# Performance work log

Hardware: AMD Instinct MI355X
Metric: run time of the kernel (lower is better)

## Reference

```python
import jax, jax.numpy as jnp
import numpy as np

B, N, C, K, S = 2, 20000, 64, 16, 4  # batch, points, channels, neighbors, share_planes
CS = C // S
EPS = 1e-5


def _gather(x, idx):
    # x: [B, C, N], idx: [B, N, K] -> [B, C, N, K]
    return jax.vmap(lambda xb, ib: xb[:, ib])(x, idx)


def _bn(x, g, b, m, v):
    # inference-mode BatchNorm2d over channel axis 1; x: [B, C, N, K]
    scale = (g / jnp.sqrt(v + EPS))[None, :, None, None]
    return (x - m[None, :, None, None]) * scale + b[None, :, None, None]


def setup_inputs() -> dict:
    key = jax.random.key(0)
    ks = jax.random.split(key, 32)
    d = {}
    d["coord"] = jax.random.normal(ks[0], (B, N, 3), jnp.float32)
    d["q"] = jax.random.normal(ks[1], (B, C, N), jnp.float32)
    d["k"] = jax.random.normal(ks[2], (B, C, N), jnp.float32)
    d["neighbor_indices"] = jax.random.randint(ks[3], (B, N, K), 0, N, jnp.int32)
    sc = 1.0 / np.sqrt(C)
    d["wq"] = jax.random.normal(ks[4], (C, C), jnp.float32) * sc
    d["bq"] = jnp.zeros((C,), jnp.float32)
    d["wk"] = jax.random.normal(ks[5], (C, C), jnp.float32) * sc
    d["bk"] = jnp.zeros((C,), jnp.float32)
    d["wv"] = jax.random.normal(ks[6], (C, C), jnp.float32) * sc
    d["bv"] = jnp.zeros((C,), jnp.float32)
    # linear_p: Conv2d(3,3,1) -> BN(3) -> ReLU -> Conv2d(3,C,1)
    d["p1_w"] = jax.random.normal(ks[7], (3, 3), jnp.float32) * 0.5
    d["p1_b"] = jnp.zeros((3,), jnp.float32)
    d["p_bn_g"] = jnp.ones((3,), jnp.float32)
    d["p_bn_b"] = jnp.zeros((3,), jnp.float32)
    d["p_bn_m"] = jax.random.normal(ks[8], (3,), jnp.float32) * 0.1
    d["p_bn_v"] = jax.random.uniform(ks[9], (3,), jnp.float32) + 0.5
    d["p2_w"] = jax.random.normal(ks[10], (C, 3), jnp.float32) * 0.5
    d["p2_b"] = jnp.zeros((C,), jnp.float32)
    # linear_w: BN(C) -> ReLU -> Conv2d(C, C//S, 1) -> BN(C//S) -> ReLU -> Conv2d(C//S, C//S, 1)
    d["w_bn1_g"] = jnp.ones((C,), jnp.float32)
    d["w_bn1_b"] = jnp.zeros((C,), jnp.float32)
    d["w_bn1_m"] = jax.random.normal(ks[11], (C,), jnp.float32) * 0.1
    d["w_bn1_v"] = jax.random.uniform(ks[12], (C,), jnp.float32) + 0.5
    d["w1_w"] = jax.random.normal(ks[13], (CS, C), jnp.float32) * sc
    d["w1_b"] = jnp.zeros((CS,), jnp.float32)
    d["w_bn2_g"] = jnp.ones((CS,), jnp.float32)
    d["w_bn2_b"] = jnp.zeros((CS,), jnp.float32)
    d["w_bn2_m"] = jax.random.normal(ks[14], (CS,), jnp.float32) * 0.1
    d["w_bn2_v"] = jax.random.uniform(ks[15], (CS,), jnp.float32) + 0.5
    d["w2_w"] = jax.random.normal(ks[16], (CS, CS), jnp.float32) / np.sqrt(CS)
    d["w2_b"] = jnp.zeros((CS,), jnp.float32)
    return d


def reference(coord, q, k, neighbor_indices, wq, bq, wk, bk, wv, bv,
              p1_w, p1_b, p_bn_g, p_bn_b, p_bn_m, p_bn_v, p2_w, p2_b,
              w_bn1_g, w_bn1_b, w_bn1_m, w_bn1_v, w1_w, w1_b,
              w_bn2_g, w_bn2_b, w_bn2_m, w_bn2_v, w2_w, w2_b):
    # 1x1 Conv1d projections: [B, C, N]
    x_q = jnp.einsum('oc,bcn->bon', wq, q) + bq[None, :, None]
    x_k = jnp.einsum('oc,bcn->bon', wk, k) + bk[None, :, None]
    x_v = jnp.einsum('oc,bcn->bon', wv, q) + bv[None, :, None]
    # KNN gathers -> [B, *, N, K]
    p_r = _gather(jnp.swapaxes(coord, 1, 2), neighbor_indices)  # [B, 3, N, K]
    x_k = _gather(x_k, neighbor_indices)                        # [B, C, N, K]
    x_v = _gather(x_v, neighbor_indices)                        # [B, C, N, K]
    # positional MLP
    p_r = jnp.einsum('oc,bcnk->bonk', p1_w, p_r) + p1_b[None, :, None, None]
    p_r = jax.nn.relu(_bn(p_r, p_bn_g, p_bn_b, p_bn_m, p_bn_v))
    p_r = jnp.einsum('oc,bcnk->bonk', p2_w, p_r) + p2_b[None, :, None, None]  # [B, C, N, K]
    # attention weights MLP
    w = x_k - x_q[:, :, :, None] + p_r                          # [B, C, N, K]
    w = jax.nn.relu(_bn(w, w_bn1_g, w_bn1_b, w_bn1_m, w_bn1_v))
    w = jnp.einsum('oc,bcnk->bonk', w1_w, w) + w1_b[None, :, None, None]      # [B, C/S, N, K]
    w = jax.nn.relu(_bn(w, w_bn2_g, w_bn2_b, w_bn2_m, w_bn2_v))
    w = jnp.einsum('oc,bcnk->bonk', w2_w, w) + w2_b[None, :, None, None]
    w = jax.nn.softmax(w, axis=-1)                              # softmax over K
    # grouped weighted sum
    v = jnp.transpose(x_v + p_r, (0, 2, 3, 1)).reshape(B, N, K, S, CS)  # [B, N, K, S, C/S]
    wp = jnp.transpose(w, (0, 2, 3, 1))                                  # [B, N, K, C/S]
    x = jnp.einsum('bnksg,bnkg->bnsg', v, wp).reshape(B, N, C)
    return jnp.transpose(x, (0, 2, 1))  # [B, C, N]
```

## Files before the change

kernel.cpp:

```cpp
#include <hip/hip_runtime.h>
#include <hip/hip_bf16.h>
#include <math.h>

#define B_ 2
#define N_ 20000
#define C_ 64
#define K_ 16
#define CS_ 16
#define EPS_ 1e-5f

typedef float f32x4_t  __attribute__((ext_vector_type(4)));
typedef short bf16x8_t __attribute__((ext_vector_type(8)));
typedef short bf16x4_t __attribute__((ext_vector_type(4)));

__device__ __forceinline__ unsigned int packbf2(float a, float b)
{
    union { __hip_bfloat162 h; unsigned int u; } cv;
    cv.h = __float22bfloat162_rn(float2{a, b});
    return cv.u;
}
__device__ __forceinline__ float bf_lo(unsigned int w)
{
    return __builtin_bit_cast(float, w << 16);
}
__device__ __forceinline__ float bf_hi(unsigned int w)
{
    return __builtin_bit_cast(float, w & 0xFFFF0000u);
}
__device__ __forceinline__ void wave_fence()
{
    __builtin_amdgcn_wave_barrier();
}

__device__ __forceinline__ float row_sum16(float x)
{
    float s = x;
    s += __builtin_bit_cast(float, __builtin_amdgcn_update_dpp(
            0, __builtin_bit_cast(int, s), 0x128, 0xF, 0xF, false));
    s += __builtin_bit_cast(float, __builtin_amdgcn_update_dpp(
            0, __builtin_bit_cast(int, s), 0x124, 0xF, 0xF, false));
    s += __builtin_bit_cast(float, __builtin_amdgcn_update_dpp(
            0, __builtin_bit_cast(int, s), 0x122, 0xF, 0xF, false));
    s += __builtin_bit_cast(float, __builtin_amdgcn_update_dpp(
            0, __builtin_bit_cast(int, s), 0x121, 0xF, 0xF, false));
    return s;
}

__global__ __launch_bounds__(256) void setup_kernel(
    const float* __restrict__ wq, const float* __restrict__ wk,
    const float* __restrict__ wv,
    const float* __restrict__ bq, const float* __restrict__ bk,
    const float* __restrict__ bv,
    const float* __restrict__ w1_w, const float* __restrict__ w1_b,
    const float* __restrict__ w2_w, const float* __restrict__ w2_b,
    const float* __restrict__ w_bn1_g, const float* __restrict__ w_bn1_b,
    const float* __restrict__ w_bn1_m, const float* __restrict__ w_bn1_v,
    const float* __restrict__ w_bn2_g, const float* __restrict__ w_bn2_b,
    const float* __restrict__ w_bn2_m, const float* __restrict__ w_bn2_v,
    const float* __restrict__ p2_w, const float* __restrict__ p2_b,
    uint4* __restrict__ wtab, uint4* __restrict__ a1tab,
    uint2* __restrict__ a2tab, float* __restrict__ cz,
    float4* __restrict__ ctab, float4* __restrict__ ptab)
{
    const int t   = threadIdx.x;
    const int blk = blockIdx.x;
    {
        int e = blk * 256 + t;
        int m = e >> 9, rem = e & 511;
        int og = rem >> 7, half = (rem >> 6) & 1, l = rem & 63;
        const float* W = (m == 0) ? wq : ((m == 1) ? wk : wv);
        const float* base = W + (size_t)(og * 16 + (l & 15)) * C_ + half * 32 + (l >> 4) * 8;
        uint4 o;
        o.x = packbf2(base[0], base[1]); o.y = packbf2(base[2], base[3]);
        o.z = packbf2(base[4], base[5]); o.w = packbf2(base[6], base[7]);
        wtab[e] = o;
    }
    if (blk == 0 && t < 128) {
        int half = t >> 6, l = t & 63;
        const float* base = w1_w + (size_t)(l & 15) * C_ + half * 32 + (l >> 4) * 8;
        uint4 o;
        o.x = packbf2(base[0], base[1]); o.y = packbf2(base[2], base[3]);
        o.z = packbf2(base[4], base[5]); o.w = packbf2(base[6], base[7]);
        a1tab[t] = o;
    }
    if (blk == 1 && t < 64) {
        const float* base = w2_w + (t & 15) * 16 + (t >> 4) * 4;
        uint2 o;
        o.x = packbf2(base[0], base[1]); o.y = packbf2(base[2], base[3]);
        a2tab[t] = o;
    }
    if (blk == 2 && t < 16) {
        float s = w_bn2_g[t] * rsqrtf(w_bn2_v[t] + EPS_);
        cz[t]      = s;
        cz[16 + t] = (w1_b[t] - w_bn2_m[t]) * s + w_bn2_b[t];
        cz[32 + t] = w2_b[t];
    }
    if (blk == 3 && t < 64) {
        float s   = w_bn1_g[t] * rsqrtf(w_bn1_v[t] + EPS_);
        float b1f = w_bn1_b[t] - w_bn1_m[t] * s;
        ctab[t] = float4{s, s * bq[t] - b1f, bk[t], bv[t]};
    }
    if (blk == 4 && t < 64) {
        ptab[t] = float4{p2_w[t*3+0], p2_w[t*3+1], p2_w[t*3+2], p2_b[t]};
    }
}

__global__ __launch_bounds__(256) void proj_kernel(
    const float* __restrict__ q, const float* __restrict__ kin,
    const float* __restrict__ coord,
    const float* __restrict__ p1_w, const float* __restrict__ p1_b,
    const float* __restrict__ p_bn_g, const float* __restrict__ p_bn_b,
    const float* __restrict__ p_bn_m, const float* __restrict__ p_bn_v,
    const uint4* __restrict__ wtab,
    const float4* __restrict__ ctab, const float4* __restrict__ ptab,
    unsigned int* __restrict__ xq2, unsigned int* __restrict__ kv_t)
{
    constexpr int PS = 26;
    __shared__ unsigned int qp[32 * PS];
    __shared__ unsigned int kp[32 * PS];

    const int t   = threadIdx.x;
    const int og  = __builtin_amdgcn_readfirstlane(t >> 6);
    const int l   = t & 63;
    const int col = l & 15;
    const int qd  = l >> 4;
    const int pt0 = blockIdx.x * 16;
    const int pt  = pt0 + col;
    const int b   = pt0 / N_;
    const int n   = pt - b * N_;
    const size_t cb = (size_t)b * C_ * N_ + n;

#pragma unroll
    for (int r = 0; r < 2; r++) {
        int cp = (og << 3) + (qd << 1) + r;
        int ci = cp * 2;
        float q0 = q[cb + (size_t)ci * N_];
        float q1 = q[cb + (size_t)(ci + 1) * N_];
        float k0 = kin[cb + (size_t)ci * N_];
        float k1 = kin[cb + (size_t)(ci + 1) * N_];
        qp[cp * PS + col] = packbf2(q0, q1);
        kp[cp * PS + col] = packbf2(k0, k1);
    }

    union bf8u { bf16x8_t v; uint4 u4; };
    bf8u awq[2], awk[2], awv[2];
#pragma unroll
    for (int half = 0; half < 2; half++) {
        awq[half].u4 = wtab[0 * 512 + og * 128 + half * 64 + l];
        awk[half].u4 = wtab[1 * 512 + og * 128 + half * 64 + l];
        awv[half].u4 = wtab[2 * 512 + og * 128 + half * 64 + l];
    }

    __syncthreads();

    union bf8b { bf16x8_t v; unsigned int u[4]; };
    bf8b bq_[2], bk_[2];
#pragma unroll
    for (int half = 0; half < 2; half++) {
#pragma unroll
        for (int i2 = 0; i2 < 4; i2++) {
            int cp = half * 16 + qd * 4 + i2;
            bq_[half].u[i2] = qp[cp * PS + col];
            bk_[half].u[i2] = kp[cp * PS + col];
        }
    }

    f32x4_t uq = {0.f, 0.f, 0.f, 0.f};
    f32x4_t uv = {0.f, 0.f, 0.f, 0.f};
    f32x4_t uk = {0.f, 0.f, 0.f, 0.f};
    uq = __builtin_amdgcn_mfma_f32_16x16x32_bf16(awq[0].v, bq_[0].v, uq, 0, 0, 0);
    uq = __builtin_amdgcn_mfma_f32_16x16x32_bf16(awq[1].v, bq_[1].v, uq, 0, 0, 0);
    uv = __builtin_amdgcn_mfma_f32_16x16x32_bf16(awv[0].v, bq_[0].v, uv, 0, 0, 0);
    uv = __builtin_amdgcn_mfma_f32_16x16x32_bf16(awv[1].v, bq_[1].v, uv, 0, 0, 0);
    uk = __builtin_amdgcn_mfma_f32_16x16x32_bf16(awk[0].v, bk_[0].v, uk, 0, 0, 0);
    uk = __builtin_amdgcn_mfma_f32_16x16x32_bf16(awk[1].v, bk_[1].v, uk, 0, 0, 0);

    float pbs[3], pbb[3];
#pragma unroll
    for (int j = 0; j < 3; j++) {
        float s = p_bn_g[j] * rsqrtf(p_bn_v[j] + EPS_);
        pbs[j] = s;
        pbb[j] = (p1_b[j] - p_bn_m[j]) * s + p_bn_b[j];
    }
    float cx = coord[pt * 3 + 0], cy = coord[pt * 3 + 1], cz = coord[pt * 3 + 2];
    float h0 = fmaxf(0.f, (p1_w[0]*cx + p1_w[1]*cy + p1_w[2]*cz) * pbs[0] + pbb[0]);
    float h1 = fmaxf(0.f, (p1_w[3]*cx + p1_w[4]*cy + p1_w[5]*cz) * pbs[1] + pbb[1]);
    float h2 = fmaxf(0.f, (p1_w[6]*cx + p1_w[7]*cy + p1_w[8]*cz) * pbs[2] + pbb[2]);

    const int ch0 = og * 16 + qd * 4;
    float xv2[4];
    uint4 kvo;
#pragma unroll
    for (int rr = 0; rr < 4; rr++) {
        const float4 ct  = ctab[ch0 + rr];
        const float4 pt4 = ptab[ch0 + rr];
        float pos = fmaf(pt4.x, h0, fmaf(pt4.y, h1, fmaf(pt4.z, h2, pt4.w)));
        xv2[rr]   = fmaf(ct.x, uq[rr], ct.y);
        float kk  = ct.x * (uk[rr] + ct.z + pos);
        float vv  = uv[rr] + ct.w + pos;
        (&kvo.x)[rr] = packbf2(kk, vv);
    }
    uint2 xqo;
    xqo.x = packbf2(xv2[0], xv2[1]);
    xqo.y = packbf2(xv2[2], xv2[3]);
    *reinterpret_cast<uint2*>(xq2 + (size_t)pt * 32 + (ch0 >> 1)) = xqo;
    *reinterpret_cast<uint4*>(kv_t + (size_t)pt * C_ + ch0) = kvo;
}

#define WROW 72
#define WPN  (K_ * WROW)
#define SS4  20
#define SPN  (K_ * SS4)
#define OS   68

__global__ __launch_bounds__(512, 8) void attn_kernel(
    const int* __restrict__ nbr,
    const unsigned int* __restrict__ xq2, const unsigned int* __restrict__ kv_t,
    const uint4* __restrict__ a1tab, const uint2* __restrict__ a2tab,
    const float* __restrict__ cz,
    float* __restrict__ out)
{
    __shared__ unsigned short wlds_all[8 * WPN];
    __shared__ float          sfb_all[8 * SPN];
    __shared__ float          otile[8 * OS];

    const int t  = threadIdx.x;
    const int w  = __builtin_amdgcn_readfirstlane(t >> 6);
    const int l  = t & 63;
    const int al = l & 15;
    const int qd = l >> 4;
    const int cquad = al;
    const int kq    = qd;
    const int c0    = cquad * 4;
    const int g0    = c0 & 15;

    const int pt0 = blockIdx.x * 8;
    const int b   = pt0 / N_;
    const int bB  = b * N_;
    const int bn  = pt0 + w;

    unsigned short* wlds = wlds_all + w * WPN;
    float*          sfb  = sfb_all + w * SPN;

    const int* nb = nbr + (size_t)bn * K_;
    uint4 kvw[4];
#pragma unroll
    for (int j = 0; j < 4; j++) {
        int idx = nb[kq * 4 + j];
        kvw[j] = *reinterpret_cast<const uint4*>(kv_t + ((size_t)(bB + idx) * C_ + c0));
    }
    const uint2 xqu = *reinterpret_cast<const uint2*>(xq2 + (size_t)bn * 32 + (c0 >> 1));
    const float xqa = bf_lo(xqu.x), xqb = bf_hi(xqu.x);
    const float xqc = bf_lo(xqu.y), xqd = bf_hi(xqu.y);

    union bf8u { bf16x8_t v; uint4 u4; };
    union bf4u { bf16x4_t v; uint2 u2; };
    bf8u a1q0, a1q1; bf4u a2q;
    a1q0.u4 = a1tab[l];
    a1q1.u4 = a1tab[64 + l];
    a2q.u2  = a2tab[l];
    const float4 zsc4 = *reinterpret_cast<const float4*>(cz + qd * 4);
    const float4 zbi4 = *reinterpret_cast<const float4*>(cz + 16 + qd * 4);
    const float4 tbi4 = *reinterpret_cast<const float4*>(cz + 32 + qd * 4);

#pragma unroll
    for (int j = 0; j < 4; j++) {
        float w0 = fmaxf(0.f, bf_lo(kvw[j].x) - xqa);
        float w1 = fmaxf(0.f, bf_lo(kvw[j].y) - xqb);
        float w2 = fmaxf(0.f, bf_lo(kvw[j].z) - xqc);
        float w3 = fmaxf(0.f, bf_lo(kvw[j].w) - xqd);
        uint2 wpk;
        wpk.x = packbf2(w0, w1);
        wpk.y = packbf2(w2, w3);
        *reinterpret_cast<uint2*>(wlds + (kq * 4 + j) * WROW + c0) = wpk;
    }
    wave_fence();

    const bf16x8_t b0 = *reinterpret_cast<const bf16x8_t*>(wlds + al * WROW + qd * 8);
    const bf16x8_t b1 = *reinterpret_cast<const bf16x8_t*>(wlds + al * WROW + 32 + qd * 8);
    f32x4_t u = {0.f, 0.f, 0.f, 0.f};
    u = __builtin_amdgcn_mfma_f32_16x16x32_bf16(a1q0.v, b0, u, 0, 0, 0);
    u = __builtin_amdgcn_mfma_f32_16x16x32_bf16(a1q1.v, b1, u, 0, 0, 0);

    union { bf16x4_t v; unsigned int u2[2]; } zb;
    {
        float z0 = fmaxf(0.f, u[0] * zsc4.x + zbi4.x);
        float z1 = fmaxf(0.f, u[1] * zsc4.y + zbi4.y);
        float z2 = fmaxf(0.f, u[2] * zsc4.z + zbi4.z);
        float z3 = fmaxf(0.f, u[3] * zsc4.w + zbi4.w);
        zb.u2[0] = packbf2(z0, z1);
        zb.u2[1] = packbf2(z2, z3);
    }

    f32x4_t t4 = {0.f, 0.f, 0.f, 0.f};
    t4 = __builtin_amdgcn_mfma_f32_16x16x16bf16_1k(a2q.v, zb.v, t4, 0, 0, 0);

    float4 sv;
#pragma unroll
    for (int rr = 0; rr < 4; rr++) {
        float e = __expf(t4[rr] + (&tbi4.x)[rr]);
        float s = row_sum16(e);
        (&sv.x)[rr] = e * __builtin_amdgcn_rcpf(s);
    }
    *reinterpret_cast<float4*>(sfb + al * SS4 + qd * 4) = sv;
    wave_fence();

    float acc[4] = {0.f, 0.f, 0.f, 0.f};
#pragma unroll
    for (int j = 0; j < 4; j++) {
        const float4 sp = *reinterpret_cast<const float4*>(sfb + (kq * 4 + j) * SS4 + g0);
        acc[0] = fmaf(bf_hi(kvw[j].x), sp.x, acc[0]);
        acc[1] = fmaf(bf_hi(kvw[j].y), sp.y, acc[1]);
        acc[2] = fmaf(bf_hi(kvw[j].z), sp.z, acc[2]);
        acc[3] = fmaf(bf_hi(kvw[j].w), sp.w, acc[3]);
    }
#pragma unroll
    for (int i = 0; i < 4; i++) {
        acc[i] += __shfl_xor(acc[i], 16);
        acc[i] += __shfl_xor(acc[i], 32);
    }
    if (kq == 0) {
        float4 o4 = float4{acc[0], acc[1], acc[2], acc[3]};
        *reinterpret_cast<float4*>(otile + w * OS + c0) = o4;
    }
    __syncthreads();

    {
        int c  = t >> 3;
        int nn = t & 7;
        out[(size_t)b * C_ * N_ + (size_t)c * N_ + (pt0 - bB) + nn] = otile[nn * OS + c];
    }
}

extern "C" void kernel_launch(void* const* d_in, const int* in_sizes, int n_in,
                              void* d_out, int out_size, void* d_ws, size_t ws_size,
                              hipStream_t stream)
{
    const float* coord = (const float*)d_in[0];
    const float* q     = (const float*)d_in[1];
    const float* k     = (const float*)d_in[2];
    const int*   nbr   = (const int*)d_in[3];
    const float* wq = (const float*)d_in[4];
    const float* bq = (const float*)d_in[5];
    const float* wk = (const float*)d_in[6];
    const float* bk = (const float*)d_in[7];
    const float* wv = (const float*)d_in[8];
    const float* bv = (const float*)d_in[9];
    const float* p1_w = (const float*)d_in[10];
    const float* p1_b = (const float*)d_in[11];
    const float* p_bn_g = (const float*)d_in[12];
    const float* p_bn_b = (const float*)d_in[13];
    const float* p_bn_m = (const float*)d_in[14];
    const float* p_bn_v = (const float*)d_in[15];
    const float* p2_w = (const float*)d_in[16];
    const float* p2_b = (const float*)d_in[17];
    const float* w_bn1_g = (const float*)d_in[18];
    const float* w_bn1_b = (const float*)d_in[19];
    const float* w_bn1_m = (const float*)d_in[20];
    const float* w_bn1_v = (const float*)d_in[21];
    const float* w1_w = (const float*)d_in[22];
    const float* w1_b = (const float*)d_in[23];
    const float* w_bn2_g = (const float*)d_in[24];
    const float* w_bn2_b = (const float*)d_in[25];
    const float* w_bn2_m = (const float*)d_in[26];
    const float* w_bn2_v = (const float*)d_in[27];
    const float* w2_w = (const float*)d_in[28];
    const float* w2_b = (const float*)d_in[29];

    const size_t PTS = (size_t)B_ * N_;
    char* wsb = (char*)d_ws;
    unsigned int* kv_t = (unsigned int*)wsb;
    unsigned int* xq2  = (unsigned int*)(wsb + PTS * C_ * 4);
    uint4* wtab  = (uint4*)(wsb + PTS * C_ * 4 + PTS * C_ * 2);
    uint4* a1tab = wtab + 1536;
    uint2* a2tab = (uint2*)(a1tab + 128);
    float* cz    = (float*)(a2tab + 64);
    float4* ctab = (float4*)(cz + 48);
    float4* ptab = ctab + 64;

    setup_kernel<<<6, 256, 0, stream>>>(
        wq, wk, wv, bq, bk, bv, w1_w, w1_b, w2_w, w2_b,
        w_bn1_g, w_bn1_b, w_bn1_m, w_bn1_v,
        w_bn2_g, w_bn2_b, w_bn2_m, w_bn2_v,
        p2_w, p2_b,
        wtab, a1tab, a2tab, cz, ctab, ptab);

    proj_kernel<<<(B_ * N_) / 16, 256, 0, stream>>>(
        q, k, coord,
        p1_w, p1_b, p_bn_g, p_bn_b, p_bn_m, p_bn_v,
        wtab, ctab, ptab, xq2, kv_t);

    attn_kernel<<<(B_ * N_) / 8, 512, 0, stream>>>(
        nbr, xq2, kv_t, a1tab, a2tab, cz,
        (float*)d_out);
}
```

Before: 44.66 us.

## Fold setup kernel into projection kernel and use DPP quad reduction

Removes the separate setup kernel. The projection kernel now reads fp32 weights directly, converts them to bf16 in registers, and computes the BN folding inline. An extra block writes the small tables the attention kernel needs. This saves one launch and its serialization, at the cost of redundant weight conversion in every block. The attention kernel's lane mapping also changes so the K-group reduction runs as an in-quad DPP sum instead of cross-row shuffles.

```diff
diff --git a/kernel.cpp b/kernel.cpp
--- a/kernel.cpp
+++ b/kernel.cpp
@@ -45,81 +45,67 @@
             0, __builtin_bit_cast(int, s), 0x121, 0xF, 0xF, false));
     return s;
 }
-
-__global__ __launch_bounds__(256) void setup_kernel(
+__device__ __forceinline__ float quad_sum4(float x)
+{
+    float s = x;
+    s += __builtin_bit_cast(float, __builtin_amdgcn_update_dpp(
+            0, __builtin_bit_cast(int, s), 0xB1, 0xF, 0xF, false));
+    s += __builtin_bit_cast(float, __builtin_amdgcn_update_dpp(
+            0, __builtin_bit_cast(int, s), 0x4E, 0xF, 0xF, false));
+    return s;
+}
+
+__global__ __launch_bounds__(256) void proj_kernel(
+    const float* __restrict__ q, const float* __restrict__ kin,
+    const float* __restrict__ coord,
     const float* __restrict__ wq, const float* __restrict__ wk,
     const float* __restrict__ wv,
     const float* __restrict__ bq, const float* __restrict__ bk,
     const float* __restrict__ bv,
-    const float* __restrict__ w1_w, const float* __restrict__ w1_b,
-    const float* __restrict__ w2_w, const float* __restrict__ w2_b,
-    const float* __restrict__ w_bn1_g, const float* __restrict__ w_bn1_b,
-    const float* __restrict__ w_bn1_m, const float* __restrict__ w_bn1_v,
-    const float* __restrict__ w_bn2_g, const float* __restrict__ w_bn2_b,
-    const float* __restrict__ w_bn2_m, const float* __restrict__ w_bn2_v,
-    const float* __restrict__ p2_w, const float* __restrict__ p2_b,
-    uint4* __restrict__ wtab, uint4* __restrict__ a1tab,
-    uint2* __restrict__ a2tab, float* __restrict__ cz,
-    float4* __restrict__ ctab, float4* __restrict__ ptab)
-{
-    const int t   = threadIdx.x;
-    const int blk = blockIdx.x;
-    {
-        int e = blk * 256 + t;
-        int m = e >> 9, rem = e & 511;
-        int og = rem >> 7, half = (rem >> 6) & 1, l = rem & 63;
-        const float* W = (m == 0) ? wq : ((m == 1) ? wk : wv);
-        const float* base = W + (size_t)(og * 16 + (l & 15)) * C_ + half * 32 + (l >> 4) * 8;
-        uint4 o;
-        o.x = packbf2(base[0], base[1]); o.y = packbf2(base[2], base[3]);
-        o.z = packbf2(base[4], base[5]); o.w = packbf2(base[6], base[7]);
-        wtab[e] = o;
-    }
-    if (blk == 0 && t < 128) {
-        int half = t >> 6, l = t & 63;
-        const float* base = w1_w + (size_t)(l & 15) * C_ + half * 32 + (l >> 4) * 8;
-        uint4 o;
-        o.x = packbf2(base[0], base[1]); o.y = packbf2(base[2], base[3]);
-        o.z = packbf2(base[4], base[5]); o.w = packbf2(base[6], base[7]);
-        a1tab[t] = o;
-    }
-    if (blk == 1 && t < 64) {
-        const float* base = w2_w + (t & 15) * 16 + (t >> 4) * 4;
-        uint2 o;
-        o.x = packbf2(base[0], base[1]); o.y = packbf2(base[2], base[3]);
-        a2tab[t] = o;
-    }
-    if (blk == 2 && t < 16) {
-        float s = w_bn2_g[t] * rsqrtf(w_bn2_v[t] + EPS_);
-        cz[t]      = s;
-        cz[16 + t] = (w1_b[t] - w_bn2_m[t]) * s + w_bn2_b[t];
-        cz[32 + t] = w2_b[t];
-    }
-    if (blk == 3 && t < 64) {
-        float s   = w_bn1_g[t] * rsqrtf(w_bn1_v[t] + EPS_);
-        float b1f = w_bn1_b[t] - w_bn1_m[t] * s;
-        ctab[t] = float4{s, s * bq[t] - b1f, bk[t], bv[t]};
-    }
-    if (blk == 4 && t < 64) {
-        ptab[t] = float4{p2_w[t*3+0], p2_w[t*3+1], p2_w[t*3+2], p2_b[t]};
-    }
-}
-
-__global__ __launch_bounds__(256) void proj_kernel(
-    const float* __restrict__ q, const float* __restrict__ kin,
-    const float* __restrict__ coord,
     const float* __restrict__ p1_w, const float* __restrict__ p1_b,
     const float* __restrict__ p_bn_g, const float* __restrict__ p_bn_b,
     const float* __restrict__ p_bn_m, const float* __restrict__ p_bn_v,
-    const uint4* __restrict__ wtab,
-    const float4* __restrict__ ctab, const float4* __restrict__ ptab,
+    const float* __restrict__ p2_w, const float* __restrict__ p2_b,
+    const float* __restrict__ w_bn1_g, const float* __restrict__ w_bn1_b,
+    const float* __restrict__ w_bn1_m, const float* __restrict__ w_bn1_v,
+    const float* __restrict__ w1_w, const float* __restrict__ w1_b,
+    const float* __restrict__ w2_w, const float* __restrict__ w2_b,
+    const float* __restrict__ w_bn2_g, const float* __restrict__ w_bn2_b,
+    const float* __restrict__ w_bn2_m, const float* __restrict__ w_bn2_v,
+    uint4* __restrict__ a1tab, uint2* __restrict__ a2tab,
+    float* __restrict__ cz,
     unsigned int* __restrict__ xq2, unsigned int* __restrict__ kv_t)
 {
+    const int t = threadIdx.x;
+
+    if (blockIdx.x == 2500) {
+        if (t < 128) {
+            int half = t >> 6, l = t & 63;
+            const float* base = w1_w + (size_t)(l & 15) * C_ + half * 32 + (l >> 4) * 8;
+            uint4 o;
+            o.x = packbf2(base[0], base[1]); o.y = packbf2(base[2], base[3]);
+            o.z = packbf2(base[4], base[5]); o.w = packbf2(base[6], base[7]);
+            a1tab[t] = o;
+        }
+        if (t < 64) {
+            const float* base = w2_w + (t & 15) * 16 + (t >> 4) * 4;
+            uint2 o;
+            o.x = packbf2(base[0], base[1]); o.y = packbf2(base[2], base[3]);
+            a2tab[t] = o;
+        }
+        if (t < 16) {
+            float s = w_bn2_g[t] * rsqrtf(w_bn2_v[t] + EPS_);
+            cz[t]      = s;
+            cz[16 + t] = (w1_b[t] - w_bn2_m[t]) * s + w_bn2_b[t];
+            cz[32 + t] = w2_b[t];
+        }
+        return;
+    }
+
     constexpr int PS = 26;
     __shared__ unsigned int qp[32 * PS];
     __shared__ unsigned int kp[32 * PS];
 
-    const int t   = threadIdx.x;
     const int og  = __builtin_amdgcn_readfirstlane(t >> 6);
     const int l   = t & 63;
     const int col = l & 15;
@@ -142,19 +128,32 @@
         kp[cp * PS + col] = packbf2(k0, k1);
     }
 
-    union bf8u { bf16x8_t v; uint4 u4; };
+    union bf8u { bf16x8_t v; uint4 u4; unsigned int u[4]; };
+    const int arow = og * 16 + col;
     bf8u awq[2], awk[2], awv[2];
 #pragma unroll
     for (int half = 0; half < 2; half++) {
-        awq[half].u4 = wtab[0 * 512 + og * 128 + half * 64 + l];
-        awk[half].u4 = wtab[1 * 512 + og * 128 + half * 64 + l];
-        awv[half].u4 = wtab[2 * 512 + og * 128 + half * 64 + l];
+        const float* wqb = wq + (size_t)arow * C_ + half * 32 + qd * 8;
+        const float* wkb = wk + (size_t)arow * C_ + half * 32 + qd * 8;
+        const float* wvb = wv + (size_t)arow * C_ + half * 32 + qd * 8;
+        float4 f0, f1;
+        f0 = *reinterpret_cast<const float4*>(wqb);
+        f1 = *reinterpret_cast<const float4*>(wqb + 4);
+        awq[half].u4 = uint4{packbf2(f0.x, f0.y), packbf2(f0.z, f0.w),
+                             packbf2(f1.x, f1.y), packbf2(f1.z, f1.w)};
+        f0 = *reinterpret_cast<const float4*>(wkb);
+        f1 = *reinterpret_cast<const float4*>(wkb + 4);
+        awk[half].u4 = uint4{packbf2(f0.x, f0.y), packbf2(f0.z, f0.w),
+                             packbf2(f1.x, f1.y), packbf2(f1.z, f1.w)};
+        f0 = *reinterpret_cast<const float4*>(wvb);
+        f1 = *reinterpret_cast<const float4*>(wvb + 4);
+        awv[half].u4 = uint4{packbf2(f0.x, f0.y), packbf2(f0.z, f0.w),
+                             packbf2(f1.x, f1.y), packbf2(f1.z, f1.w)};
     }
 
     __syncthreads();
 
-    union bf8b { bf16x8_t v; unsigned int u[4]; };
-    bf8b bq_[2], bk_[2];
+    bf8u bq_[2], bk_[2];
 #pragma unroll
     for (int half = 0; half < 2; half++) {
 #pragma unroll
@@ -182,22 +181,39 @@
         pbs[j] = s;
         pbb[j] = (p1_b[j] - p_bn_m[j]) * s + p_bn_b[j];
     }
-    float cx = coord[pt * 3 + 0], cy = coord[pt * 3 + 1], cz = coord[pt * 3 + 2];
-    float h0 = fmaxf(0.f, (p1_w[0]*cx + p1_w[1]*cy + p1_w[2]*cz) * pbs[0] + pbb[0]);
-    float h1 = fmaxf(0.f, (p1_w[3]*cx + p1_w[4]*cy + p1_w[5]*cz) * pbs[1] + pbb[1]);
-    float h2 = fmaxf(0.f, (p1_w[6]*cx + p1_w[7]*cy + p1_w[8]*cz) * pbs[2] + pbb[2]);
+    float cx = coord[pt * 3 + 0], cy = coord[pt * 3 + 1], cz_ = coord[pt * 3 + 2];
+    float h0 = fmaxf(0.f, (p1_w[0]*cx + p1_w[1]*cy + p1_w[2]*cz_) * pbs[0] + pbb[0]);
+    float h1 = fmaxf(0.f, (p1_w[3]*cx + p1_w[4]*cy + p1_w[5]*cz_) * pbs[1] + pbb[1]);
+    float h2 = fmaxf(0.f, (p1_w[6]*cx + p1_w[7]*cy + p1_w[8]*cz_) * pbs[2] + pbb[2]);
 
     const int ch0 = og * 16 + qd * 4;
+    const float4 g1  = *reinterpret_cast<const float4*>(w_bn1_g + ch0);
+    const float4 b1  = *reinterpret_cast<const float4*>(w_bn1_b + ch0);
+    const float4 m1  = *reinterpret_cast<const float4*>(w_bn1_m + ch0);
+    const float4 v1  = *reinterpret_cast<const float4*>(w_bn1_v + ch0);
+    const float4 bqv = *reinterpret_cast<const float4*>(bq + ch0);
+    const float4 bkv = *reinterpret_cast<const float4*>(bk + ch0);
+    const float4 bvv = *reinterpret_cast<const float4*>(bv + ch0);
+    const float4 pw0 = *reinterpret_cast<const float4*>(p2_w + (size_t)ch0 * 3);
+    const float4 pw1 = *reinterpret_cast<const float4*>(p2_w + (size_t)ch0 * 3 + 4);
+    const float4 pw2 = *reinterpret_cast<const float4*>(p2_w + (size_t)ch0 * 3 + 8);
+    const float4 pb4 = *reinterpret_cast<const float4*>(p2_b + ch0);
+
+    float pos[4];
+    pos[0] = fmaf(pw0.x, h0, fmaf(pw0.y, h1, fmaf(pw0.z, h2, pb4.x)));
+    pos[1] = fmaf(pw0.w, h0, fmaf(pw1.x, h1, fmaf(pw1.y, h2, pb4.y)));
+    pos[2] = fmaf(pw1.z, h0, fmaf(pw1.w, h1, fmaf(pw2.x, h2, pb4.z)));
+    pos[3] = fmaf(pw2.y, h0, fmaf(pw2.z, h1, fmaf(pw2.w, h2, pb4.w)));
+
     float xv2[4];
     uint4 kvo;
 #pragma unroll
     for (int rr = 0; rr < 4; rr++) {
-        const float4 ct  = ctab[ch0 + rr];
-        const float4 pt4 = ptab[ch0 + rr];
-        float pos = fmaf(pt4.x, h0, fmaf(pt4.y, h1, fmaf(pt4.z, h2, pt4.w)));
-        xv2[rr]   = fmaf(ct.x, uq[rr], ct.y);
-        float kk  = ct.x * (uk[rr] + ct.z + pos);
-        float vv  = uv[rr] + ct.w + pos;
+        float s   = (&g1.x)[rr] * rsqrtf((&v1.x)[rr] + EPS_);
+        float b1f = (&b1.x)[rr] - (&m1.x)[rr] * s;
+        xv2[rr]   = s * (uq[rr] + (&bqv.x)[rr]) - b1f;
+        float kk  = s * (uk[rr] + (&bkv.x)[rr] + pos[rr]);
+        float vv  = uv[rr] + (&bvv.x)[rr] + pos[rr];
         (&kvo.x)[rr] = packbf2(kk, vv);
     }
     uint2 xqo;
@@ -229,8 +245,8 @@
     const int l  = t & 63;
     const int al = l & 15;
     const int qd = l >> 4;
-    const int cquad = al;
-    const int kq    = qd;
+    const int cquad = l >> 2;
+    const int kq    = l & 3;
     const int c0    = cquad * 4;
     const int g0    = c0 & 15;
 
@@ -315,10 +331,8 @@
         acc[3] = fmaf(bf_hi(kvw[j].w), sp.w, acc[3]);
     }
 #pragma unroll
-    for (int i = 0; i < 4; i++) {
-        acc[i] += __shfl_xor(acc[i], 16);
-        acc[i] += __shfl_xor(acc[i], 32);
-    }
+    for (int i = 0; i < 4; i++)
+        acc[i] = quad_sum4(acc[i]);
     if (kq == 0) {
         float4 o4 = float4{acc[0], acc[1], acc[2], acc[3]};
         *reinterpret_cast<float4*>(otile + w * OS + c0) = o4;
@@ -371,24 +385,17 @@
     char* wsb = (char*)d_ws;
     unsigned int* kv_t = (unsigned int*)wsb;
     unsigned int* xq2  = (unsigned int*)(wsb + PTS * C_ * 4);
-    uint4* wtab  = (uint4*)(wsb + PTS * C_ * 4 + PTS * C_ * 2);
-    uint4* a1tab = wtab + 1536;
+    uint4* a1tab = (uint4*)(wsb + PTS * C_ * 4 + PTS * C_ * 2);
     uint2* a2tab = (uint2*)(a1tab + 128);
     float* cz    = (float*)(a2tab + 64);
-    float4* ctab = (float4*)(cz + 48);
-    float4* ptab = ctab + 64;
-
-    setup_kernel<<<6, 256, 0, stream>>>(
-        wq, wk, wv, bq, bk, bv, w1_w, w1_b, w2_w, w2_b,
+
+    proj_kernel<<<2501, 256, 0, stream>>>(
+        q, k, coord, wq, wk, wv, bq, bk, bv,
+        p1_w, p1_b, p_bn_g, p_bn_b, p_bn_m, p_bn_v, p2_w, p2_b,
         w_bn1_g, w_bn1_b, w_bn1_m, w_bn1_v,
+        w1_w, w1_b, w2_w, w2_b,
         w_bn2_g, w_bn2_b, w_bn2_m, w_bn2_v,
-        p2_w, p2_b,
-        wtab, a1tab, a2tab, cz, ctab, ptab);
-
-    proj_kernel<<<(B_ * N_) / 16, 256, 0, stream>>>(
-        q, k, coord,
-        p1_w, p1_b, p_bn_g, p_bn_b, p_bn_m, p_bn_v,
-        wtab, ctab, ptab, xq2, kv_t);
+        a1tab, a2tab, cz, xq2, kv_t);
 
     attn_kernel<<<(B_ * N_) / 8, 512, 0, stream>>>(
         nbr, xq2, kv_t, a1tab, a2tab, cz,
```

Result: slower. 62.33 us (+39.6%).
